# Kernel optimization log

Hardware: AMD Instinct MI355X
Metric: run time of the kernel (lower is better)

## Reference

```python
import jax, jax.numpy as jnp
import numpy as np

NUM_ELEM = 62
DEGREE = 3
M = 64  # matrix_size = sqrt(layer_sizes[0]) = sqrt(4096)
IN_DIM, H = 4096, 2048
N_POINTS = 2_097_152


def _glorot(k, shape):
    lim = np.float32(np.sqrt(2.0 / (shape[0] + shape[1])))
    return jax.random.normal(k, shape, jnp.float32) * lim


def setup_inputs() -> dict:
    key = jax.random.key(0)
    ks = jax.random.split(key, 4)
    points = jax.random.uniform(ks[0], (N_POINTS, 2), jnp.float32)
    # first coordinate lives in [-1, 1) (original maps it via (x+1)/2)
    points = points.at[:, 0].set(points[:, 0] * 2.0 - 1.0)
    return {
        "points": points,
        "W1": _glorot(ks[1], (IN_DIM, H)), "b1": jnp.zeros((H,), jnp.float32),
        "W2": _glorot(ks[2], (H, H)),      "b2": jnp.zeros((H,), jnp.float32),
        "W3": _glorot(ks[3], (H, 1)),      "b3": jnp.zeros((1,), jnp.float32),
    }


def _quadratic(t):
    # tfg bspline._quadratic: 3 quadratic B-spline basis functions of t in [0,1)
    return jnp.stack([(1.0 - t) ** 2 * 0.5, -t * t + t + 0.5, t * t * 0.5], axis=-1)


def _spline(coord):
    p = coord * NUM_ELEM
    pos = jnp.minimum(jnp.floor(p).astype(jnp.int32) + 1, NUM_ELEM)  # tf.cond clamp
    return _quadratic(jnp.mod(p, 1.0)), pos


def reference(points, W1, b1, W2, b2, W3, b3):
    # cofs = eye(4096); identity @ W1 == W1, so the first Dense reduces to W1 + b1
    h = jnp.tanh(W1 + b1)
    h = jnp.tanh(h @ W2 + b2)
    out = jnp.tanh(h @ W3 + b3)          # [4096, 1]
    u = out.reshape(M, M) * 3.0           # control-point grid [64, 64]

    x = (points[:, 0] + 1.0) * 0.5
    y = points[:, 1]
    bx, px = _spline(x)                   # bx: [N,3], px: [N]
    by, py = _spline(y)
    offs = jnp.arange(DEGREE)
    ix = px[:, None] - 1 + offs           # [N,3] row indices into u
    iy = py[:, None] - 1 + offs           # [N,3] col indices into u
    Wn = u[ix[:, :, None], iy[:, None, :]]  # [N,3,3] local control-point windows
    # sum_{i,j} W[i,j] * splines_x[i] * splines_y[j]  (meshgrid orientation)
    return jnp.einsum('nij,ni,nj->n', Wn, bx, by)
```

## Files before the change

kernel.cpp:

```cpp
#include <hip/hip_runtime.h>
#include <stdint.h>

#define IN_DIM 4096
#define H_DIM  2048
#define NPTS   2097152

typedef short  bf16x8  __attribute__((ext_vector_type(8)));
typedef float  floatx4 __attribute__((ext_vector_type(4)));

#define AS1 __attribute__((address_space(1)))
#define AS3 __attribute__((address_space(3)))

__device__ __forceinline__ unsigned short f2bf(float f) {
    unsigned u = __float_as_uint(f);
    unsigned r = (u + 0x7FFFu + ((u >> 16) & 1u)) >> 16;
    return (unsigned short)r;
}

__global__ void prep_all(const float* __restrict__ W1, const float* __restrict__ b1,
                         const float* __restrict__ W2,
                         unsigned short* __restrict__ hbf, unsigned short* __restrict__ W2T,
                         float* __restrict__ rowsum) {
    __shared__ unsigned short tile[64][66];
    int b = blockIdx.x;
    if (b < 8192) {
        if (b < 16) rowsum[b * 256 + threadIdx.x] = 0.0f;
        int idx = (b * 256 + threadIdx.x) * 4;
        float4 w = *(const float4*)(W1 + idx);
        float4 bb = *(const float4*)(b1 + (idx & (H_DIM - 1)));
        ushort4 o;
        o.x = f2bf(tanhf(w.x + bb.x));
        o.y = f2bf(tanhf(w.y + bb.y));
        o.z = f2bf(tanhf(w.z + bb.z));
        o.w = f2bf(tanhf(w.w + bb.w));
        *(ushort4*)(hbf + idx) = o;
    } else {
        int bb = b - 8192;
        int k0 = (bb >> 5) * 64, n0 = (bb & 31) * 64;
        for (int idx = threadIdx.x; idx < 64 * 64; idx += 256) {
            int r = idx >> 6, c = idx & 63;
            tile[c][r] = f2bf(W2[(size_t)(k0 + r) * H_DIM + n0 + c]);
        }
        __syncthreads();
        for (int idx = threadIdx.x; idx < 64 * 64; idx += 256) {
            int r = idx >> 6, c = idx & 63;
            W2T[(size_t)(n0 + r) * H_DIM + k0 + c] = tile[r][c];
        }
    }
}

#define BK 64
__global__ __launch_bounds__(256, 4) void gemm_fused(
    const unsigned short* __restrict__ A,
    const unsigned short* __restrict__ BT,
    const float* __restrict__ b2, const float* __restrict__ W3,
    float* __restrict__ rowsum) {
    __shared__ __align__(16) unsigned short As[128 * BK];
    __shared__ __align__(16) unsigned short Bs[64 * BK];
    const int K = H_DIM;
    const int t = threadIdx.x;
    const int w = t >> 6, l = t & 63;
    const int lane16 = l & 15, quad = l >> 4;
    const int wr = w >> 1, wc = w & 1;
    const int rowBase = blockIdx.y * 128;
    const int colBase = blockIdx.x * 64;

    const int sRow = l >> 3;
    const int sChunk = (l & 7) ^ sRow;
    const size_t laneOff = (size_t)sRow * K + sChunk * 8;

    const unsigned short* aBase = A  + (size_t)(rowBase + w * 32) * K + laneOff;
    const unsigned short* bBase = BT + (size_t)(colBase + w * 16) * K + laneOff;

    floatx4 acc[4][2];
    floatx4 zero = {0.f, 0.f, 0.f, 0.f};
#pragma unroll
    for (int i = 0; i < 4; ++i)
#pragma unroll
        for (int j = 0; j < 2; ++j) acc[i][j] = zero;

    for (int k0 = 0; k0 < K; k0 += BK) {
        __syncthreads();
#pragma unroll
        for (int i = 0; i < 4; ++i)
            __builtin_amdgcn_global_load_lds(
                (const AS1 void*)(aBase + (size_t)i * 8 * K + k0),
                (AS3 void*)(As + (w * 32 + i * 8) * 64), 16, 0, 0);
#pragma unroll
        for (int i = 0; i < 2; ++i)
            __builtin_amdgcn_global_load_lds(
                (const AS1 void*)(bBase + (size_t)i * 8 * K + k0),
                (AS3 void*)(Bs + (w * 16 + i * 8) * 64), 16, 0, 0);
        __syncthreads();

#pragma unroll
        for (int s = 0; s < 2; ++s) {
            const int cs = (s * 4 + quad) ^ (lane16 & 7);
            bf16x8 af[4], bfr[2];
#pragma unroll
            for (int mi = 0; mi < 4; ++mi)
                af[mi] = *(const bf16x8*)(As + (wr * 64 + mi * 16 + lane16) * 64 + cs * 8);
#pragma unroll
            for (int ni = 0; ni < 2; ++ni)
                bfr[ni] = *(const bf16x8*)(Bs + (wc * 32 + ni * 16 + lane16) * 64 + cs * 8);
#pragma unroll
            for (int mi = 0; mi < 4; ++mi)
#pragma unroll
                for (int ni = 0; ni < 2; ++ni)
                    acc[mi][ni] = __builtin_amdgcn_mfma_f32_16x16x32_bf16(
                        af[mi], bfr[ni], acc[mi][ni], 0, 0, 0);
        }
    }

    const int rowG = rowBase + wr * 64;
#pragma unroll
    for (int mi = 0; mi < 4; ++mi) {
#pragma unroll
        for (int r = 0; r < 4; ++r) {
            float s = 0.f;
#pragma unroll
            for (int ni = 0; ni < 2; ++ni) {
                int col = colBase + wc * 32 + ni * 16 + lane16;
                float v = acc[mi][ni][r] + b2[col];
                s += tanhf(v) * W3[col];
            }
#pragma unroll
            for (int off = 1; off < 16; off <<= 1) s += __shfl_xor(s, off, 64);
            if (lane16 == 0)
                atomicAdd(&rowsum[rowG + mi * 16 + quad * 4 + r], s);
        }
    }
}

__device__ __forceinline__ float spline_eval(const float* us, float ptx, float pty) {
    float x = (ptx + 1.0f) * 0.5f;
    float px = x * 62.0f, py = pty * 62.0f;
    float fx = floorf(px), fy = floorf(py);
    int posx = min((int)fx + 1, 62);
    int posy = min((int)fy + 1, 62);
    float tx = px - fx, ty = py - fy;
    float bx0 = 0.5f * (1.f - tx) * (1.f - tx);
    float bx1 = -tx * tx + tx + 0.5f;
    float bx2 = 0.5f * tx * tx;
    float by0 = 0.5f * (1.f - ty) * (1.f - ty);
    float by1 = -ty * ty + ty + 0.5f;
    float by2 = 0.5f * ty * ty;
    const float* r0 = &us[(posx - 1) * 64 + (posy - 1)];
    const float* r1 = r0 + 64;
    const float* r2 = r1 + 64;
    float s0 = r0[0] * by0 + r0[1] * by1 + r0[2] * by2;
    float s1 = r1[0] * by0 + r1[1] * by1 + r1[2] * by2;
    float s2 = r2[0] * by0 + r2[1] * by1 + r2[2] * by2;
    return bx0 * s0 + bx1 * s1 + bx2 * s2;
}

__global__ void spline_kernel(const float4* __restrict__ pts,
                              const float* __restrict__ rowsum,
                              const float* __restrict__ b3,
                              float2* __restrict__ out, int npairs) {
    __shared__ float us[4096];
    float bias = b3[0];
    for (int i = threadIdx.x; i < 4096; i += blockDim.x)
        us[i] = 3.0f * tanhf(rowsum[i] + bias);
    __syncthreads();
    int stride = gridDim.x * blockDim.x;
    for (int idx = blockIdx.x * blockDim.x + threadIdx.x; idx < npairs; idx += stride) {
        float4 p2 = pts[idx];
        float2 o;
        o.x = spline_eval(us, p2.x, p2.y);
        o.y = spline_eval(us, p2.z, p2.w);
        out[idx] = o;
    }
}

extern "C" void kernel_launch(void* const* d_in, const int* in_sizes, int n_in,
                              void* d_out, int out_size, void* d_ws, size_t ws_size,
                              hipStream_t stream) {
    const float* points = (const float*)d_in[0];
    const float* W1 = (const float*)d_in[1];
    const float* b1 = (const float*)d_in[2];
    const float* W2 = (const float*)d_in[3];
    const float* b2 = (const float*)d_in[4];
    const float* W3 = (const float*)d_in[5];
    const float* b3 = (const float*)d_in[6];
    float* out = (float*)d_out;

    char* ws = (char*)d_ws;
    unsigned short* hbf = (unsigned short*)ws;
    unsigned short* w2t = (unsigned short*)(ws + 16777216);
    float* rowsum = (float*)(ws + 25165824);

    prep_all<<<8192 + 1024, 256, 0, stream>>>(W1, b1, W2, hbf, w2t, rowsum);
    gemm_fused<<<dim3(H_DIM / 64, IN_DIM / 128), 256, 0, stream>>>(hbf, w2t, b2, W3, rowsum);
    spline_kernel<<<1024, 256, 0, stream>>>((const float4*)points, rowsum, b3,
                                            (float2*)out, NPTS / 2);
}
```

Before: 168.2 us.

## Double-buffer LDS tiles in the bf16 GEMM to overlap loads with MFMA

Splits the A and B shared-memory tiles into two buffers and restructures the K loop so the next tile's global-to-LDS load is issued before the MFMAs on the current tile run. Each step now needs one barrier, preceded by a vmcnt wait, instead of two. This is meant to hide global-load latency behind the matrix math. In exchange, LDS use doubles and the launch-bounds occupancy hint drops from 4 to 3 blocks per CU, so fewer waves are resident to hide latency.

```diff
diff --git a/kernel.cpp b/kernel.cpp
--- a/kernel.cpp
+++ b/kernel.cpp
@@ -50,13 +50,15 @@
 }
 
 #define BK 64
-__global__ __launch_bounds__(256, 4) void gemm_fused(
+__global__ __launch_bounds__(256, 3) void gemm_fused(
     const unsigned short* __restrict__ A,
     const unsigned short* __restrict__ BT,
     const float* __restrict__ b2, const float* __restrict__ W3,
     float* __restrict__ rowsum) {
-    __shared__ __align__(16) unsigned short As[128 * BK];
-    __shared__ __align__(16) unsigned short Bs[64 * BK];
+    __shared__ __align__(16) unsigned short As0[128 * BK];
+    __shared__ __align__(16) unsigned short As1[128 * BK];
+    __shared__ __align__(16) unsigned short Bs0[64 * BK];
+    __shared__ __align__(16) unsigned short Bs1[64 * BK];
     const int K = H_DIM;
     const int t = threadIdx.x;
     const int w = t >> 6, l = t & 63;
@@ -79,38 +81,64 @@
 #pragma unroll
         for (int j = 0; j < 2; ++j) acc[i][j] = zero;
 
-    for (int k0 = 0; k0 < K; k0 += BK) {
-        __syncthreads();
-#pragma unroll
-        for (int i = 0; i < 4; ++i)
-            __builtin_amdgcn_global_load_lds(
-                (const AS1 void*)(aBase + (size_t)i * 8 * K + k0),
-                (AS3 void*)(As + (w * 32 + i * 8) * 64), 16, 0, 0);
-#pragma unroll
-        for (int i = 0; i < 2; ++i)
-            __builtin_amdgcn_global_load_lds(
-                (const AS1 void*)(bBase + (size_t)i * 8 * K + k0),
-                (AS3 void*)(Bs + (w * 16 + i * 8) * 64), 16, 0, 0);
-        __syncthreads();
-
-#pragma unroll
-        for (int s = 0; s < 2; ++s) {
-            const int cs = (s * 4 + quad) ^ (lane16 & 7);
-            bf16x8 af[4], bfr[2];
-#pragma unroll
-            for (int mi = 0; mi < 4; ++mi)
-                af[mi] = *(const bf16x8*)(As + (wr * 64 + mi * 16 + lane16) * 64 + cs * 8);
-#pragma unroll
-            for (int ni = 0; ni < 2; ++ni)
-                bfr[ni] = *(const bf16x8*)(Bs + (wc * 32 + ni * 16 + lane16) * 64 + cs * 8);
-#pragma unroll
-            for (int mi = 0; mi < 4; ++mi)
-#pragma unroll
-                for (int ni = 0; ni < 2; ++ni)
-                    acc[mi][ni] = __builtin_amdgcn_mfma_f32_16x16x32_bf16(
-                        af[mi], bfr[ni], acc[mi][ni], 0, 0, 0);
-        }
-    }
+#define STAGE(AsB, BsB, k0)                                                    \
+    {                                                                          \
+        _Pragma("unroll")                                                      \
+        for (int i = 0; i < 4; ++i)                                            \
+            __builtin_amdgcn_global_load_lds(                                  \
+                (const AS1 void*)(aBase + (size_t)i * 8 * K + (k0)),           \
+                (AS3 void*)(AsB + (w * 32 + i * 8) * 64), 16, 0, 0);           \
+        _Pragma("unroll")                                                      \
+        for (int i = 0; i < 2; ++i)                                            \
+            __builtin_amdgcn_global_load_lds(                                  \
+                (const AS1 void*)(bBase + (size_t)i * 8 * K + (k0)),           \
+                (AS3 void*)(BsB + (w * 16 + i * 8) * 64), 16, 0, 0);           \
+    }
+
+#define COMPUTE(AsB, BsB)                                                      \
+    {                                                                          \
+        _Pragma("unroll")                                                      \
+        for (int s = 0; s < 2; ++s) {                                          \
+            const int cs = (s * 4 + quad) ^ (lane16 & 7);                      \
+            bf16x8 af[4], bfr[2];                                              \
+            _Pragma("unroll")                                                  \
+            for (int mi = 0; mi < 4; ++mi)                                     \
+                af[mi] = *(const bf16x8*)(AsB + (wr * 64 + mi * 16 + lane16) * 64 + cs * 8); \
+            _Pragma("unroll")                                                  \
+            for (int ni = 0; ni < 2; ++ni)                                     \
+                bfr[ni] = *(const bf16x8*)(BsB + (wc * 32 + ni * 16 + lane16) * 64 + cs * 8); \
+            _Pragma("unroll")                                                  \
+            for (int mi = 0; mi < 4; ++mi)                                     \
+                _Pragma("unroll")                                              \
+                for (int ni = 0; ni < 2; ++ni)                                 \
+                    acc[mi][ni] = __builtin_amdgcn_mfma_f32_16x16x32_bf16(     \
+                        af[mi], bfr[ni], acc[mi][ni], 0, 0, 0);                \
+        }                                                                      \
+    }
+
+#define SYNC()                                                                 \
+    asm volatile("s_waitcnt vmcnt(0)" ::: "memory");                           \
+    __builtin_amdgcn_s_barrier();
+
+    STAGE(As0, Bs0, 0);
+    SYNC();
+
+    for (int k0 = BK; k0 < 31 * BK; k0 += 2 * BK) {
+        STAGE(As1, Bs1, k0);
+        COMPUTE(As0, Bs0);
+        SYNC();
+        STAGE(As0, Bs0, k0 + BK);
+        COMPUTE(As1, Bs1);
+        SYNC();
+    }
+    STAGE(As1, Bs1, 31 * BK);
+    COMPUTE(As0, Bs0);
+    SYNC();
+    COMPUTE(As1, Bs1);
+
+#undef STAGE
+#undef COMPUTE
+#undef SYNC
 
     const int rowG = rowBase + wr * 64;
 #pragma unroll
```

New measurement: 182.1 us. 1.08x slower.
